# Optimization experiments

Measured on AMD Instinct MI355X. Metric: run time of the kernel, lower is better.

The kernel has to match this reference:

```python
import jax, jax.numpy as jnp
import numpy as np

ROUTING = 3
IN_RES = 1152
NUM_CLASSES = 10
BATCH = 512


def squash(s):
    # s: [B, C, 16]; v = (|s|^2 / (1+|s|^2)) * s/|s|  == |s|/(1+|s|^2) * s
    square_sum = jnp.sum(s * s, axis=2)          # [B, C]
    norm = jnp.sqrt(square_sum)                  # [B, C]
    factor = square_sum / (norm * (1.0 + square_sum))
    return factor[:, :, None] * s


def setup_inputs() -> dict:
    key = jax.random.key(0)
    k1, k2 = jax.random.split(key)
    u = jax.random.normal(k1, (BATCH, IN_RES, 8), dtype=jnp.float32)
    W = jax.random.normal(k2, (1, IN_RES, NUM_CLASSES, 8, 16), dtype=jnp.float32)
    return {"u": u, "W": W}


def reference(u, W):
    # u: [B, R, 8], W: [1, R, C, 8, 16]
    # u_hat[b,r,c,o] = sum_i u[b,r,i] * W[0,r,c,i,o]  -> [B, R, C, 16]
    u_hat = jnp.einsum('bri,rcio->brco', u, W[0])
    B = u.shape[0]
    b = jnp.zeros((B, IN_RES, NUM_CLASSES, 1), dtype=u.dtype)
    v = None
    for _ in range(ROUTING):
        c = jax.nn.softmax(b, axis=2)            # softmax over classes
        s = jnp.sum(u_hat * c, axis=1)           # [B, C, 16]
        v = squash(s)                            # [B, C, 16]
        b = b + jnp.sum(u_hat * v[:, None], axis=3, keepdims=True)
    return v
```

## Files before the change

kernel.cpp:

```cpp
#include <hip/hip_runtime.h>
#include <hip/hip_bf16.h>


#define NBATCH 512
#define NR     1152
#define NCLS   10
#define NOUT   16
#define RCHUNK 18
#define NPX    64
#define CO     160

__device__ __forceinline__ unsigned short f2bf_rne(float x) {
    unsigned u = __float_as_uint(x);
    return (unsigned short)((u + 0x7fffu + ((u >> 16) & 1u)) >> 16);
}

template<bool FIRST>
__global__ __launch_bounds__(256, 2)
void caps_pass(const float* __restrict__ U, const float* __restrict__ W,
               const float* __restrict__ Vsum, float* __restrict__ Pg)
{
    __shared__ float s_part[64][161];
    __shared__ unsigned short vs_l[64][162];

    const int tid  = threadIdx.x;
    const int lane = tid & 63;
    const int b0   = ((int)blockIdx.y) << 6;

    for (int idx = tid; idx < 64 * 161; idx += 256)
        (&s_part[0][0])[idx] = 0.0f;
    if (!FIRST) {
        for (int idx = tid; idx < 64 * CO; idx += 256) {
            int bl = idx / CO;
            int m  = idx - bl * CO;
            vs_l[bl][m] = f2bf_rne(Vsum[(size_t)(b0 + bl) * CO + m]);
        }
    }
    __syncthreads();

    const int wv    = __builtin_amdgcn_readfirstlane(tid >> 6);
    const int rbase = (int)blockIdx.x * RCHUNK;
    const size_t ubase = (size_t)(b0 + lane) * (NR * 8);

    for (int r = rbase + wv; r < rbase + RCHUNK; r += 4) {
        const float4* up = reinterpret_cast<const float4*>(U + ubase + (size_t)r * 8);
        float4 u0 = up[0], u1 = up[1];
        const float uu[8] = {u0.x,u0.y,u0.z,u0.w, u1.x,u1.y,u1.z,u1.w};

        const float* wr = W + (size_t)r * (NCLS * 128);

        float uh[NCLS][NOUT];
        #pragma unroll
        for (int c = 0; c < NCLS; ++c) {
            #pragma unroll
            for (int o = 0; o < NOUT; ++o) uh[c][o] = 0.0f;
            #pragma unroll
            for (int i = 0; i < 8; ++i) {
                const float4* wp = reinterpret_cast<const float4*>(wr + c * 128 + i * 16);
                float4 w0 = wp[0], w1 = wp[1], w2 = wp[2], w3 = wp[3];
                const float wf[16] = {w0.x,w0.y,w0.z,w0.w, w1.x,w1.y,w1.z,w1.w,
                                      w2.x,w2.y,w2.z,w2.w, w3.x,w3.y,w3.z,w3.w};
                const float ui = uu[i];
                #pragma unroll
                for (int o = 0; o < NOUT; ++o)
                    uh[c][o] = __builtin_fmaf(ui, wf[o], uh[c][o]);
            }
        }

        float coef[NCLS];
        if (FIRST) {
            #pragma unroll
            for (int c = 0; c < NCLS; ++c) coef[c] = 0.1f;
        } else {
            float lg[NCLS];
            #pragma unroll
            for (int c = 0; c < NCLS; ++c) {
                float acc = 0.0f;
                #pragma unroll
                for (int o2 = 0; o2 < 8; ++o2) {
                    const unsigned pv =
                        *reinterpret_cast<const unsigned*>(&vs_l[lane][c * 16 + o2 * 2]);
                    acc = __builtin_fmaf(uh[c][o2*2],     __uint_as_float(pv << 16), acc);
                    acc = __builtin_fmaf(uh[c][o2*2 + 1], __uint_as_float(pv & 0xffff0000u), acc);
                }
                lg[c] = acc;
            }
            float mx = lg[0];
            #pragma unroll
            for (int c = 1; c < NCLS; ++c) mx = fmaxf(mx, lg[c]);
            float den = 0.0f;
            #pragma unroll
            for (int c = 0; c < NCLS; ++c) { float e = __expf(lg[c] - mx); coef[c] = e; den += e; }
            const float inv = 1.0f / den;
            #pragma unroll
            for (int c = 0; c < NCLS; ++c) coef[c] *= inv;
        }

        #pragma unroll
        for (int c = 0; c < NCLS; ++c) {
            const float cc = coef[c];
            #pragma unroll
            for (int o = 0; o < NOUT; ++o)
                atomicAdd(&s_part[lane][c * 16 + o], cc * uh[c][o]);
        }
    }

    __syncthreads();

    float* pg = Pg + (size_t)((int)blockIdx.y * NPX + (int)blockIdx.x) * (64 * CO);
    for (int idx = tid; idx < 64 * CO; idx += 256) {
        int bl = idx / CO;
        int m  = idx - bl * CO;
        pg[idx] = s_part[bl][m];
    }
}

__global__ __launch_bounds__(256)
void caps_reduce_squash(const float* __restrict__ Pg, float* __restrict__ Vsum,
                        float* __restrict__ out, const int mode)
{
    const int g = (int)blockIdx.x * 256 + threadIdx.x;
    const int b = g / CO;
    const int m = g - b * CO;
    const int y = b >> 6, bl = b & 63;

    const float* p = Pg + ((size_t)(y * NPX) * 64 + bl) * CO + m;
    float s = 0.0f;
    #pragma unroll 16
    for (int x = 0; x < NPX; ++x)
        s += p[(size_t)x * (64 * CO)];

    float ss = s * s;
    ss += __shfl_xor(ss, 1);
    ss += __shfl_xor(ss, 2);
    ss += __shfl_xor(ss, 4);
    ss += __shfl_xor(ss, 8);
    const float f = sqrtf(ss) / (1.0f + ss);
    const float v = f * s;

    if (mode == 2)      out[g] = v;
    else if (mode == 0) Vsum[g] = v;
    else                Vsum[g] += v;
}

extern "C" void kernel_launch(void* const* d_in, const int* in_sizes, int n_in,
                              void* d_out, int out_size, void* d_ws, size_t ws_size,
                              hipStream_t stream)
{
    (void)in_sizes; (void)n_in; (void)out_size; (void)ws_size;
    const float* U = (const float*)d_in[0];
    const float* W = (const float*)d_in[1];
    float* Pg   = (float*)d_ws;
    float* Vsum = Pg + (size_t)NBATCH * NPX * CO;
    float* out  = (float*)d_out;

    dim3 grid(NR / RCHUNK, NBATCH / 64);
    dim3 blk(256);
    dim3 rgrid((NBATCH * CO) / 256);

    caps_pass<true ><<<grid, blk, 0, stream>>>(U, W, nullptr, Pg);
    caps_reduce_squash<<<rgrid, blk, 0, stream>>>(Pg, Vsum, nullptr, 0);
    caps_pass<false><<<grid, blk, 0, stream>>>(U, W, Vsum, Pg);
    caps_reduce_squash<<<rgrid, blk, 0, stream>>>(Pg, Vsum, nullptr, 1);
    caps_pass<false><<<grid, blk, 0, stream>>>(U, W, Vsum, Pg);
    caps_reduce_squash<<<rgrid, blk, 0, stream>>>(Pg, Vsum, out, 2);
}
```

Measured before the change: 1.556 ms.

## Stage W chunk in LDS, recompute u_hat per class, use 512-thread blocks

The W slice for the block's 18 routes is copied into shared memory once instead of being read from global memory by each wave. The full 10x16 u_hat register array is replaced by per-class recomputation: once for the logits and once for the weighted accumulation. This frees registers so the block can grow to 512 threads (8 waves). Vsum is packed as bf16 uint4 vectors for wide LDS reads. The cost is twice the FMA work in the non-first passes and a much larger shared memory footprint (about 92KB for W plus the existing arrays), which may limit how many blocks fit per CU. The 18 routes are now split over 8 waves, so two waves get 3 routes and the others get 2.

```diff
diff --git a/kernel.cpp b/kernel.cpp
--- a/kernel.cpp
+++ b/kernel.cpp
@@ -16,56 +16,52 @@
 }
 
 template<bool FIRST>
-__global__ __launch_bounds__(256, 2)
+__global__ __launch_bounds__(512, 2)
 void caps_pass(const float* __restrict__ U, const float* __restrict__ W,
                const float* __restrict__ Vsum, float* __restrict__ Pg)
 {
+    __shared__ float wt[RCHUNK * 1280];
     __shared__ float s_part[64][161];
-    __shared__ unsigned short vs_l[64][162];
+    __shared__ uint4 vs_sm[20 * 64];
 
     const int tid  = threadIdx.x;
     const int lane = tid & 63;
     const int b0   = ((int)blockIdx.y) << 6;
+    const int rbase = (int)blockIdx.x * RCHUNK;
 
-    for (int idx = tid; idx < 64 * 161; idx += 256)
-        (&s_part[0][0])[idx] = 0.0f;
+    {
+        const float4* Wg4 = reinterpret_cast<const float4*>(W + (size_t)rbase * 1280);
+        float4* wt4 = reinterpret_cast<float4*>(wt);
+        for (int k = tid; k < RCHUNK * 320; k += 512)
+            wt4[k] = Wg4[k];
+    }
     if (!FIRST) {
-        for (int idx = tid; idx < 64 * CO; idx += 256) {
-            int bl = idx / CO;
-            int m  = idx - bl * CO;
-            vs_l[bl][m] = f2bf_rne(Vsum[(size_t)(b0 + bl) * CO + m]);
+        for (int f = tid; f < 20 * 64; f += 512) {
+            const int k = f >> 6, l = f & 63;
+            const float* vrow = Vsum + (size_t)(b0 + l) * CO + k * 8;
+            float4 a = *reinterpret_cast<const float4*>(vrow);
+            float4 b = *reinterpret_cast<const float4*>(vrow + 4);
+            uint4 q;
+            q.x = ((unsigned)f2bf_rne(a.y) << 16) | f2bf_rne(a.x);
+            q.y = ((unsigned)f2bf_rne(a.w) << 16) | f2bf_rne(a.z);
+            q.z = ((unsigned)f2bf_rne(b.y) << 16) | f2bf_rne(b.x);
+            q.w = ((unsigned)f2bf_rne(b.w) << 16) | f2bf_rne(b.z);
+            vs_sm[f] = q;
         }
     }
+    for (int idx = tid; idx < 64 * 161; idx += 512)
+        (&s_part[0][0])[idx] = 0.0f;
     __syncthreads();
 
-    const int wv    = __builtin_amdgcn_readfirstlane(tid >> 6);
-    const int rbase = (int)blockIdx.x * RCHUNK;
+    const int wv = __builtin_amdgcn_readfirstlane(tid >> 6);
     const size_t ubase = (size_t)(b0 + lane) * (NR * 8);
 
-    for (int r = rbase + wv; r < rbase + RCHUNK; r += 4) {
+    for (int rl = wv; rl < RCHUNK; rl += 8) {
+        const int r = rbase + rl;
         const float4* up = reinterpret_cast<const float4*>(U + ubase + (size_t)r * 8);
         float4 u0 = up[0], u1 = up[1];
         const float uu[8] = {u0.x,u0.y,u0.z,u0.w, u1.x,u1.y,u1.z,u1.w};
-
-        const float* wr = W + (size_t)r * (NCLS * 128);
-
-        float uh[NCLS][NOUT];
-        #pragma unroll
-        for (int c = 0; c < NCLS; ++c) {
-            #pragma unroll
-            for (int o = 0; o < NOUT; ++o) uh[c][o] = 0.0f;
-            #pragma unroll
-            for (int i = 0; i < 8; ++i) {
-                const float4* wp = reinterpret_cast<const float4*>(wr + c * 128 + i * 16);
-                float4 w0 = wp[0], w1 = wp[1], w2 = wp[2], w3 = wp[3];
-                const float wf[16] = {w0.x,w0.y,w0.z,w0.w, w1.x,w1.y,w1.z,w1.w,
-                                      w2.x,w2.y,w2.z,w2.w, w3.x,w3.y,w3.z,w3.w};
-                const float ui = uu[i];
-                #pragma unroll
-                for (int o = 0; o < NOUT; ++o)
-                    uh[c][o] = __builtin_fmaf(ui, wf[o], uh[c][o]);
-            }
-        }
+        const float* wrow = wt + rl * 1280;
 
         float coef[NCLS];
         if (FIRST) {
@@ -75,13 +71,28 @@
             float lg[NCLS];
             #pragma unroll
             for (int c = 0; c < NCLS; ++c) {
+                float uhc[NOUT];
+                #pragma unroll
+                for (int o = 0; o < NOUT; ++o) uhc[o] = 0.0f;
+                #pragma unroll
+                for (int i = 0; i < 8; ++i) {
+                    const float4* wp = reinterpret_cast<const float4*>(wrow + c*128 + i*16);
+                    float4 w0 = wp[0], w1 = wp[1], w2 = wp[2], w3 = wp[3];
+                    const float wf[16] = {w0.x,w0.y,w0.z,w0.w, w1.x,w1.y,w1.z,w1.w,
+                                          w2.x,w2.y,w2.z,w2.w, w3.x,w3.y,w3.z,w3.w};
+                    const float ui = uu[i];
+                    #pragma unroll
+                    for (int o = 0; o < NOUT; ++o)
+                        uhc[o] = __builtin_fmaf(ui, wf[o], uhc[o]);
+                }
+                const uint4 qa = vs_sm[(c*2+0)*64 + lane];
+                const uint4 qb = vs_sm[(c*2+1)*64 + lane];
+                const unsigned pk[8] = {qa.x,qa.y,qa.z,qa.w, qb.x,qb.y,qb.z,qb.w};
                 float acc = 0.0f;
                 #pragma unroll
-                for (int o2 = 0; o2 < 8; ++o2) {
-                    const unsigned pv =
-                        *reinterpret_cast<const unsigned*>(&vs_l[lane][c * 16 + o2 * 2]);
-                    acc = __builtin_fmaf(uh[c][o2*2],     __uint_as_float(pv << 16), acc);
-                    acc = __builtin_fmaf(uh[c][o2*2 + 1], __uint_as_float(pv & 0xffff0000u), acc);
+                for (int t = 0; t < 8; ++t) {
+                    acc = __builtin_fmaf(uhc[t*2],   __uint_as_float(pk[t] << 16),        acc);
+                    acc = __builtin_fmaf(uhc[t*2+1], __uint_as_float(pk[t] & 0xffff0000u), acc);
                 }
                 lg[c] = acc;
             }
@@ -98,17 +109,31 @@
 
         #pragma unroll
         for (int c = 0; c < NCLS; ++c) {
+            float uhc[NOUT];
+            #pragma unroll
+            for (int o = 0; o < NOUT; ++o) uhc[o] = 0.0f;
+            #pragma unroll
+            for (int i = 0; i < 8; ++i) {
+                const float4* wp = reinterpret_cast<const float4*>(wrow + c*128 + i*16);
+                float4 w0 = wp[0], w1 = wp[1], w2 = wp[2], w3 = wp[3];
+                const float wf[16] = {w0.x,w0.y,w0.z,w0.w, w1.x,w1.y,w1.z,w1.w,
+                                      w2.x,w2.y,w2.z,w2.w, w3.x,w3.y,w3.z,w3.w};
+                const float ui = uu[i];
+                #pragma unroll
+                for (int o = 0; o < NOUT; ++o)
+                    uhc[o] = __builtin_fmaf(ui, wf[o], uhc[o]);
+            }
             const float cc = coef[c];
             #pragma unroll
             for (int o = 0; o < NOUT; ++o)
-                atomicAdd(&s_part[lane][c * 16 + o], cc * uh[c][o]);
+                atomicAdd(&s_part[lane][c * 16 + o], cc * uhc[o]);
         }
     }
 
     __syncthreads();
 
     float* pg = Pg + (size_t)((int)blockIdx.y * NPX + (int)blockIdx.x) * (64 * CO);
-    for (int idx = tid; idx < 64 * CO; idx += 256) {
+    for (int idx = tid; idx < 64 * CO; idx += 512) {
         int bl = idx / CO;
         int m  = idx - bl * CO;
         pg[idx] = s_part[bl][m];
@@ -155,13 +180,13 @@
     float* out  = (float*)d_out;
 
     dim3 grid(NR / RCHUNK, NBATCH / 64);
-    dim3 blk(256);
+    dim3 blk(512);
     dim3 rgrid((NBATCH * CO) / 256);
 
     caps_pass<true ><<<grid, blk, 0, stream>>>(U, W, nullptr, Pg);
-    caps_reduce_squash<<<rgrid, blk, 0, stream>>>(Pg, Vsum, nullptr, 0);
+    caps_reduce_squash<<<rgrid, 256, 0, stream>>>(Pg, Vsum, nullptr, 0);
     caps_pass<false><<<grid, blk, 0, stream>>>(U, W, Vsum, Pg);
-    caps_reduce_squash<<<rgrid, blk, 0, stream>>>(Pg, Vsum, nullptr, 1);
+    caps_reduce_squash<<<rgrid, 256, 0, stream>>>(Pg, Vsum, nullptr, 1);
     caps_pass<false><<<grid, blk, 0, stream>>>(U, W, Vsum, Pg);
-    caps_reduce_squash<<<rgrid, blk, 0, stream>>>(Pg, Vsum, out, 2);
+    caps_reduce_squash<<<rgrid, 256, 0, stream>>>(Pg, Vsum, out, 2);
 }
```

Result: slower. 4.881 ms (+213.6%).

## Stage W in LDS, use 1024-thread blocks and recompute u_hat per class

Applied to the files above, without the earlier changes.

Each caps_pass block now copies its chunk of W into shared memory and runs 16 waves instead of 4. The full 160-float u_hat register array is replaced by a per-class loop: a first pass computes logits with an online softmax, and a second pass recomputes u_hat for each class and adds it into shared memory. V is pre-packed into bf16 uint4 vectors so it loads as one vector. The aim is to cut register pressure and global W traffic and raise occupancy, at the cost of computing u_hat twice and using more LDS per block.

```diff
diff --git a/kernel.cpp b/kernel.cpp
--- a/kernel.cpp
+++ b/kernel.cpp
@@ -1,133 +1,169 @@
 #include <hip/hip_runtime.h>
-#include <hip/hip_bf16.h>
 
 
 #define NBATCH 512
 #define NR     1152
 #define NCLS   10
 #define NOUT   16
-#define RCHUNK 18
-#define NPX    64
 #define CO     160
 
 __device__ __forceinline__ unsigned short f2bf_rne(float x) {
     unsigned u = __float_as_uint(x);
     return (unsigned short)((u + 0x7fffu + ((u >> 16) & 1u)) >> 16);
 }
-
-template<bool FIRST>
-__global__ __launch_bounds__(256, 2)
+__device__ __forceinline__ unsigned pack2(float lo, float hi) {
+    return ((unsigned)f2bf_rne(hi) << 16) | f2bf_rne(lo);
+}
+__device__ __forceinline__ float bflo(unsigned q) { return __uint_as_float(q << 16); }
+__device__ __forceinline__ float bfhi(unsigned q) { return __uint_as_float(q & 0xffff0000u); }
+
+__device__ __forceinline__ float4 fma4(float s, float4 w, float4 a) {
+    a.x = __builtin_fmaf(s, w.x, a.x);
+    a.y = __builtin_fmaf(s, w.y, a.y);
+    a.z = __builtin_fmaf(s, w.z, a.z);
+    a.w = __builtin_fmaf(s, w.w, a.w);
+    return a;
+}
+__device__ __forceinline__ float dot8(float4 a, float4 b, uint4 q, float acc) {
+    acc = __builtin_fmaf(a.x, bflo(q.x), acc);
+    acc = __builtin_fmaf(a.y, bfhi(q.x), acc);
+    acc = __builtin_fmaf(a.z, bflo(q.y), acc);
+    acc = __builtin_fmaf(a.w, bfhi(q.y), acc);
+    acc = __builtin_fmaf(b.x, bflo(q.z), acc);
+    acc = __builtin_fmaf(b.y, bfhi(q.z), acc);
+    acc = __builtin_fmaf(b.z, bflo(q.w), acc);
+    acc = __builtin_fmaf(b.w, bfhi(q.w), acc);
+    return acc;
+}
+
+template<int RCH, bool FIRST>
+__global__ __launch_bounds__(1024, 4)
 void caps_pass(const float* __restrict__ U, const float* __restrict__ W,
-               const float* __restrict__ Vsum, float* __restrict__ Pg)
+               const float* __restrict__ Vs, float* __restrict__ Pg)
 {
+    __shared__ float wt[RCH * 1280];
     __shared__ float s_part[64][161];
-    __shared__ unsigned short vs_l[64][162];
+    __shared__ uint4 vs_sm[2 * NCLS * 64];
 
     const int tid  = threadIdx.x;
     const int lane = tid & 63;
     const int b0   = ((int)blockIdx.y) << 6;
-
-    for (int idx = tid; idx < 64 * 161; idx += 256)
+    const int rbase = (int)blockIdx.x * RCH;
+
+    {
+        const float4* Wg4 = reinterpret_cast<const float4*>(W + (size_t)rbase * 1280);
+        float4* wt4 = reinterpret_cast<float4*>(wt);
+        for (int k = tid; k < RCH * 320; k += 1024)
+            wt4[k] = Wg4[k];
+    }
+    if (!FIRST) {
+        for (int f = tid; f < 2 * NCLS * 64; f += 1024) {
+            const int k = f >> 6, l = f & 63;
+            const float* vrow = Vs + (size_t)(b0 + l) * CO + k * 8;
+            float4 a = *reinterpret_cast<const float4*>(vrow);
+            float4 b = *reinterpret_cast<const float4*>(vrow + 4);
+            uint4 q;
+            q.x = pack2(a.x, a.y);
+            q.y = pack2(a.z, a.w);
+            q.z = pack2(b.x, b.y);
+            q.w = pack2(b.z, b.w);
+            vs_sm[f] = q;
+        }
+    }
+    for (int idx = tid; idx < 64 * 161; idx += 1024)
         (&s_part[0][0])[idx] = 0.0f;
-    if (!FIRST) {
-        for (int idx = tid; idx < 64 * CO; idx += 256) {
-            int bl = idx / CO;
-            int m  = idx - bl * CO;
-            vs_l[bl][m] = f2bf_rne(Vsum[(size_t)(b0 + bl) * CO + m]);
+    __syncthreads();
+
+    const int wv = __builtin_amdgcn_readfirstlane(tid >> 6);
+
+    for (int rl = wv; rl < RCH; rl += 16) {
+        const float4* up = reinterpret_cast<const float4*>(
+            U + (size_t)(b0 + lane) * (NR * 8) + (size_t)(rbase + rl) * 8);
+        const float4 u0 = up[0], u1 = up[1];
+        const float uu[8] = {u0.x, u0.y, u0.z, u0.w, u1.x, u1.y, u1.z, u1.w};
+        const float4* wp = reinterpret_cast<const float4*>(wt + rl * 1280);
+
+        float m = -1e30f, inv = 0.0f;
+
+        if (!FIRST) {
+            float den = 0.0f;
+            #pragma unroll 1
+            for (int c = 0; c < NCLS; ++c) {
+                float4 A0 = {0,0,0,0}, A1 = {0,0,0,0}, A2 = {0,0,0,0}, A3 = {0,0,0,0};
+                #pragma unroll
+                for (int i = 0; i < 8; ++i) {
+                    const float ui = uu[i];
+                    A0 = fma4(ui, wp[c*32 + i*4 + 0], A0);
+                    A1 = fma4(ui, wp[c*32 + i*4 + 1], A1);
+                    A2 = fma4(ui, wp[c*32 + i*4 + 2], A2);
+                    A3 = fma4(ui, wp[c*32 + i*4 + 3], A3);
+                }
+                const uint4 qa = vs_sm[(2*c)     * 64 + lane];
+                const uint4 qb = vs_sm[(2*c + 1) * 64 + lane];
+                float lg = dot8(A0, A1, qa, 0.0f);
+                lg = dot8(A2, A3, qb, lg);
+                const float mn = fmaxf(m, lg);
+                den = den * __expf(m - mn) + __expf(lg - mn);
+                m = mn;
+            }
+            inv = 1.0f / den;
         }
-    }
-    __syncthreads();
-
-    const int wv    = __builtin_amdgcn_readfirstlane(tid >> 6);
-    const int rbase = (int)blockIdx.x * RCHUNK;
-    const size_t ubase = (size_t)(b0 + lane) * (NR * 8);
-
-    for (int r = rbase + wv; r < rbase + RCHUNK; r += 4) {
-        const float4* up = reinterpret_cast<const float4*>(U + ubase + (size_t)r * 8);
-        float4 u0 = up[0], u1 = up[1];
-        const float uu[8] = {u0.x,u0.y,u0.z,u0.w, u1.x,u1.y,u1.z,u1.w};
-
-        const float* wr = W + (size_t)r * (NCLS * 128);
-
-        float uh[NCLS][NOUT];
-        #pragma unroll
+
+        #pragma unroll 1
         for (int c = 0; c < NCLS; ++c) {
-            #pragma unroll
-            for (int o = 0; o < NOUT; ++o) uh[c][o] = 0.0f;
+            float4 A0 = {0,0,0,0}, A1 = {0,0,0,0}, A2 = {0,0,0,0}, A3 = {0,0,0,0};
             #pragma unroll
             for (int i = 0; i < 8; ++i) {
-                const float4* wp = reinterpret_cast<const float4*>(wr + c * 128 + i * 16);
-                float4 w0 = wp[0], w1 = wp[1], w2 = wp[2], w3 = wp[3];
-                const float wf[16] = {w0.x,w0.y,w0.z,w0.w, w1.x,w1.y,w1.z,w1.w,
-                                      w2.x,w2.y,w2.z,w2.w, w3.x,w3.y,w3.z,w3.w};
                 const float ui = uu[i];
-                #pragma unroll
-                for (int o = 0; o < NOUT; ++o)
-                    uh[c][o] = __builtin_fmaf(ui, wf[o], uh[c][o]);
+                A0 = fma4(ui, wp[c*32 + i*4 + 0], A0);
+                A1 = fma4(ui, wp[c*32 + i*4 + 1], A1);
+                A2 = fma4(ui, wp[c*32 + i*4 + 2], A2);
+                A3 = fma4(ui, wp[c*32 + i*4 + 3], A3);
             }
+            float cc;
+            if (FIRST) {
+                cc = 0.1f;
+            } else {
+                const uint4 qa = vs_sm[(2*c)     * 64 + lane];
+                const uint4 qb = vs_sm[(2*c + 1) * 64 + lane];
+                float lg = dot8(A0, A1, qa, 0.0f);
+                lg = dot8(A2, A3, qb, lg);
+                cc = __expf(lg - m) * inv;
+            }
+            float* sp = &s_part[lane][c * 16];
+            atomicAdd(sp + 0,  cc * A0.x);  atomicAdd(sp + 1,  cc * A0.y);
+            atomicAdd(sp + 2,  cc * A0.z);  atomicAdd(sp + 3,  cc * A0.w);
+            atomicAdd(sp + 4,  cc * A1.x);  atomicAdd(sp + 5,  cc * A1.y);
+            atomicAdd(sp + 6,  cc * A1.z);  atomicAdd(sp + 7,  cc * A1.w);
+            atomicAdd(sp + 8,  cc * A2.x);  atomicAdd(sp + 9,  cc * A2.y);
+            atomicAdd(sp + 10, cc * A2.z);  atomicAdd(sp + 11, cc * A2.w);
+            atomicAdd(sp + 12, cc * A3.x);  atomicAdd(sp + 13, cc * A3.y);
+            atomicAdd(sp + 14, cc * A3.z);  atomicAdd(sp + 15, cc * A3.w);
         }
-
-        float coef[NCLS];
-        if (FIRST) {
-            #pragma unroll
-            for (int c = 0; c < NCLS; ++c) coef[c] = 0.1f;
-        } else {
-            float lg[NCLS];
-            #pragma unroll
-            for (int c = 0; c < NCLS; ++c) {
-                float acc = 0.0f;
-                #pragma unroll
-                for (int o2 = 0; o2 < 8; ++o2) {
-                    const unsigned pv =
-                        *reinterpret_cast<const unsigned*>(&vs_l[lane][c * 16 + o2 * 2]);
-                    acc = __builtin_fmaf(uh[c][o2*2],     __uint_as_float(pv << 16), acc);
-                    acc = __builtin_fmaf(uh[c][o2*2 + 1], __uint_as_float(pv & 0xffff0000u), acc);
-                }
-                lg[c] = acc;
-            }
-            float mx = lg[0];
-            #pragma unroll
-            for (int c = 1; c < NCLS; ++c) mx = fmaxf(mx, lg[c]);
-            float den = 0.0f;
-            #pragma unroll
-            for (int c = 0; c < NCLS; ++c) { float e = __expf(lg[c] - mx); coef[c] = e; den += e; }
-            const float inv = 1.0f / den;
-            #pragma unroll
-            for (int c = 0; c < NCLS; ++c) coef[c] *= inv;
-        }
-
-        #pragma unroll
-        for (int c = 0; c < NCLS; ++c) {
-            const float cc = coef[c];
-            #pragma unroll
-            for (int o = 0; o < NOUT; ++o)
-                atomicAdd(&s_part[lane][c * 16 + o], cc * uh[c][o]);
-        }
     }
 
     __syncthreads();
 
-    float* pg = Pg + (size_t)((int)blockIdx.y * NPX + (int)blockIdx.x) * (64 * CO);
-    for (int idx = tid; idx < 64 * CO; idx += 256) {
-        int bl = idx / CO;
-        int m  = idx - bl * CO;
-        pg[idx] = s_part[bl][m];
+    float* pg = Pg + (size_t)((int)blockIdx.y * gridDim.x + (int)blockIdx.x) * (64 * CO);
+    for (int idx = tid; idx < 64 * CO; idx += 1024) {
+        const int bl = idx / CO;
+        const int mm = idx - bl * CO;
+        pg[idx] = s_part[bl][mm];
     }
 }
 
 __global__ __launch_bounds__(256)
 void caps_reduce_squash(const float* __restrict__ Pg, float* __restrict__ Vsum,
-                        float* __restrict__ out, const int mode)
+                        float* __restrict__ out, const int mode, const int npx)
 {
     const int g = (int)blockIdx.x * 256 + threadIdx.x;
     const int b = g / CO;
     const int m = g - b * CO;
     const int y = b >> 6, bl = b & 63;
 
-    const float* p = Pg + ((size_t)(y * NPX) * 64 + bl) * CO + m;
+    const float* p = Pg + ((size_t)y * npx * 64 + bl) * CO + m;
     float s = 0.0f;
-    #pragma unroll 16
-    for (int x = 0; x < NPX; ++x)
+    for (int x = 0; x < npx; ++x)
         s += p[(size_t)x * (64 * CO)];
 
     float ss = s * s;
@@ -147,21 +183,35 @@
                               void* d_out, int out_size, void* d_ws, size_t ws_size,
                               hipStream_t stream)
 {
-    (void)in_sizes; (void)n_in; (void)out_size; (void)ws_size;
+    (void)in_sizes; (void)n_in; (void)out_size;
     const float* U = (const float*)d_in[0];
     const float* W = (const float*)d_in[1];
-    float* Pg   = (float*)d_ws;
-    float* Vsum = Pg + (size_t)NBATCH * NPX * CO;
     float* out  = (float*)d_out;
-
-    dim3 grid(NR / RCHUNK, NBATCH / 64);
-    dim3 blk(256);
+    dim3 blk(1024);
     dim3 rgrid((NBATCH * CO) / 256);
 
-    caps_pass<true ><<<grid, blk, 0, stream>>>(U, W, nullptr, Pg);
-    caps_reduce_squash<<<rgrid, blk, 0, stream>>>(Pg, Vsum, nullptr, 0);
-    caps_pass<false><<<grid, blk, 0, stream>>>(U, W, Vsum, Pg);
-    caps_reduce_squash<<<rgrid, blk, 0, stream>>>(Pg, Vsum, nullptr, 1);
-    caps_pass<false><<<grid, blk, 0, stream>>>(U, W, Vsum, Pg);
-    caps_reduce_squash<<<rgrid, blk, 0, stream>>>(Pg, Vsum, out, 2);
-}
+    const size_t need72 = ((size_t)8 * 72 * 64 * CO + (size_t)NBATCH * CO) * sizeof(float);
+    if (ws_size >= need72) {
+        const int npx = 72;
+        float* Pg   = (float*)d_ws;
+        float* Vsum = Pg + (size_t)8 * npx * 64 * CO;
+        dim3 grid(npx, NBATCH / 64);
+        caps_pass<16, true ><<<grid, blk, 0, stream>>>(U, W, nullptr, Pg);
+        caps_reduce_squash<<<rgrid, 256, 0, stream>>>(Pg, Vsum, nullptr, 0, npx);
+        caps_pass<16, false><<<grid, blk, 0, stream>>>(U, W, Vsum, Pg);
+        caps_reduce_squash<<<rgrid, 256, 0, stream>>>(Pg, Vsum, nullptr, 1, npx);
+        caps_pass<16, false><<<grid, blk, 0, stream>>>(U, W, Vsum, Pg);
+        caps_reduce_squash<<<rgrid, 256, 0, stream>>>(Pg, Vsum, out, 2, npx);
+    } else {
+        const int npx = 64;
+        float* Pg   = (float*)d_ws;
+        float* Vsum = Pg + (size_t)8 * npx * 64 * CO;
+        dim3 grid(npx, NBATCH / 64);
+        caps_pass<18, true ><<<grid, blk, 0, stream>>>(U, W, nullptr, Pg);
+        caps_reduce_squash<<<rgrid, 256, 0, stream>>>(Pg, Vsum, nullptr, 0, npx);
+        caps_pass<18, false><<<grid, blk, 0, stream>>>(U, W, Vsum, Pg);
+        caps_reduce_squash<<<rgrid, 256, 0, stream>>>(Pg, Vsum, nullptr, 1, npx);
+        caps_pass<18, false><<<grid, blk, 0, stream>>>(U, W, Vsum, Pg);
+        caps_reduce_squash<<<rgrid, 256, 0, stream>>>(Pg, Vsum, out, 2, npx);
+    }
+}
```

New measurement: 2.248 ms. 1.44x slower.
